# Kernel optimization log

Hardware: AMD Instinct MI355X
Metric: run time of the kernel (lower is better)

## Reference

```python
import jax, jax.numpy as jnp
import numpy as np

N, D = 1024, 256


def setup_inputs() -> dict:
    key = jax.random.key(0)
    k1, k2, k3, k4, k5 = jax.random.split(key, 5)
    s1 = 1.0 / np.sqrt(2 * D)  # fan_in of first linear
    s2 = 1.0 / np.sqrt(D)      # fan_in of second linear
    return {
        "nodes": jax.random.normal(k1, (N, D), dtype=jnp.float32),
        "W1": jax.random.normal(k2, (D, 2 * D), dtype=jnp.float32) * s1,
        "b1": jax.random.normal(k3, (D,), dtype=jnp.float32) * s1,
        "W2": jax.random.normal(k4, (1, D), dtype=jnp.float32) * s2,
        "b2": jax.random.normal(k5, (1,), dtype=jnp.float32) * s2,
    }


def reference(nodes, W1, b1, W2, b2):
    # Original: pair = cat([n_i, n_j], -1); A = sigmoid(Linear2(relu(Linear1(pair))))
    # Algebraically: Linear1(cat(n_i, n_j)) = n_i @ Wa^T + n_j @ Wb^T + b1
    d = nodes.shape[1]
    Wa, Wb = W1[:, :d], W1[:, d:]
    a = nodes @ Wa.T  # (N, D) row-side projection
    b = nodes @ Wb.T  # (N, D) col-side projection
    h = jax.nn.relu(a[:, None, :] + b[None, :, :] + b1)  # (N, N, D)
    logits = jnp.einsum("ijd,d->ij", h, W2[0]) + b2[0]   # (N, N)
    return jax.nn.sigmoid(logits)
```

## Files before the change

### kernel.cpp

```cpp
#include <hip/hip_runtime.h>
#include <math.h>

#define N_NODES 1024
#define DIM     256

typedef float f32x2 __attribute__((ext_vector_type(2)));

__device__ __forceinline__ f32x2 relu2(f32x2 x) {
    return __builtin_elementwise_max(x, (f32x2)0.0f);
}

__global__ __launch_bounds__(256, 2) void k1_gemm(
    const float* __restrict__ nodes, const float* __restrict__ W1,
    const float* __restrict__ b1, float* __restrict__ At, float* __restrict__ Bt)
{
    __shared__ float nt[128][34];
    __shared__ f32x2 wab[DIM][17];

    const int t  = threadIdx.x;
    const int i0 = (blockIdx.x & 31) * 32;
    const int d0 = (blockIdx.x >> 5) * 16;

    {
        const int m = t & 15, s = t >> 4;
        const float* srcA = W1 + (d0 + s) * (2 * DIM);
        const float* srcB = srcA + DIM;
        #pragma unroll
        for (int rep = 0; rep < 4; ++rep) {
            const int k = rep * 64 + m * 4;
            float4 va = *(const float4*)(srcA + k);
            float4 vb = *(const float4*)(srcB + k);
            wab[k+0][s] = f32x2{va.x, vb.x};
            wab[k+1][s] = f32x2{va.y, vb.y};
            wab[k+2][s] = f32x2{va.z, vb.z};
            wab[k+3][s] = f32x2{va.w, vb.w};
        }
    }

    const int tx = t & 15;
    const int ty = t >> 4;
    const int sm = t & 7, ss = t >> 3;
    const float* nsrc = nodes + (i0 + ss) * DIM;

    f32x2 accA = {0.f, 0.f}, accB = {0.f, 0.f};

    for (int kc = 0; kc < DIM; kc += 128) {
        __syncthreads();
        #pragma unroll
        for (int rep = 0; rep < 4; ++rep) {
            const int k = rep * 32 + sm * 4;
            float4 v = *(const float4*)(nsrc + kc + k);
            nt[k+0][ss] = v.x; nt[k+1][ss] = v.y;
            nt[k+2][ss] = v.z; nt[k+3][ss] = v.w;
        }
        __syncthreads();

        #pragma unroll 8
        for (int k = 0; k < 128; ++k) {
            f32x2 av = *(const f32x2*)&nt[k][tx * 2];
            f32x2 wv = wab[kc + k][ty];
            f32x2 waa = __builtin_shufflevector(wv, wv, 0, 0);
            f32x2 wbb = __builtin_shufflevector(wv, wv, 1, 1);
            accA = __builtin_elementwise_fma(av, waa, accA);
            accB = __builtin_elementwise_fma(av, wbb, accB);
        }
    }

    const int d = d0 + ty;
    const int i = i0 + tx * 2;
    const float bb = b1[d];
    f32x2 oa = accA + f32x2{bb, bb};
    *(f32x2*)&At[d * N_NODES + i] = oa;
    *(f32x2*)&Bt[d * N_NODES + i] = accB;
}

__global__ __launch_bounds__(256, 4) void k2_pair(
    const float* __restrict__ At, const float* __restrict__ Bt,
    const float* __restrict__ W2, const float* __restrict__ b2,
    float* __restrict__ out)
{
    __shared__ float As[128][32];
    __shared__ float Bs[128][32];

    const int t  = threadIdx.x;
    const int i0 = (blockIdx.x & 31) * 32;
    const int j0 = (blockIdx.x >> 5) * 32;
    const int tx = t & 15;
    const int ty = t >> 4;

    f32x2 acc0 = {0.f, 0.f};
    f32x2 acc1 = {0.f, 0.f};

    for (int dc = 0; dc < DIM; dc += 128) {
        __syncthreads();
        #pragma unroll
        for (int rep = 0; rep < 4; ++rep) {
            const int flat = rep * 256 + t;
            const int row  = flat >> 3;
            const int c4   = (flat & 7) * 4;
            *(float4*)&As[row][c4] = *(const float4*)(At + (dc+row) * N_NODES + i0 + c4);
            *(float4*)&Bs[row][c4] = *(const float4*)(Bt + (dc+row) * N_NODES + j0 + c4);
        }
        __syncthreads();

        #pragma unroll 8
        for (int d = 0; d < 128; ++d) {
            const float w = W2[dc + d];
            f32x2 wv = {w, w};
            f32x2 a2 = *(const f32x2*)&As[d][ty * 2];
            f32x2 bj = *(const f32x2*)&Bs[d][tx * 2];
            f32x2 axx = __builtin_shufflevector(a2, a2, 0, 0);
            f32x2 ayy = __builtin_shufflevector(a2, a2, 1, 1);
            acc0 = __builtin_elementwise_fma(relu2(axx + bj), wv, acc0);
            acc1 = __builtin_elementwise_fma(relu2(ayy + bj), wv, acc1);
        }
    }

    const float bb = b2[0];
    f32x2 x0 = acc0 + f32x2{bb, bb};
    f32x2 x1 = acc1 + f32x2{bb, bb};
    float2 o0, o1;
    o0.x = 1.0f / (1.0f + __expf(-x0.x));
    o0.y = 1.0f / (1.0f + __expf(-x0.y));
    o1.x = 1.0f / (1.0f + __expf(-x1.x));
    o1.y = 1.0f / (1.0f + __expf(-x1.y));

    const int r = i0 + ty * 2;
    const int c = j0 + tx * 2;
    *(float2*)&out[(r    ) * N_NODES + c] = o0;
    *(float2*)&out[(r + 1) * N_NODES + c] = o1;
}

extern "C" void kernel_launch(void* const* d_in, const int* in_sizes, int n_in,
                              void* d_out, int out_size, void* d_ws, size_t ws_size,
                              hipStream_t stream) {
    const float* nodes = (const float*)d_in[0];
    const float* W1    = (const float*)d_in[1];
    const float* b1    = (const float*)d_in[2];
    const float* W2    = (const float*)d_in[3];
    const float* b2    = (const float*)d_in[4];
    float* out = (float*)d_out;

    float* At = (float*)d_ws;
    float* Bt = At + DIM * N_NODES;

    k1_gemm<<<512,  256, 0, stream>>>(nodes, W1, b1, At, Bt);
    k2_pair<<<1024, 256, 0, stream>>>(At, Bt, W2, b2, out);
}
```

Before: 94.11 us.

## Enlarge pairwise kernel tile to 64x64 with 4x4 outputs per thread

The pairwise relu-reduction kernel now gives each thread a 4x4 block of outputs and each block a 64x64 tile, loaded from LDS as float4 vectors. Each A and B value loaded is reused across more outputs, which lowers LDS traffic per FMA. Output stores widen to float4. The grid shrinks to 256 blocks, roughly one per CU, and the occupancy hint is dropped. That reduces the number of waves available to hide latency.

```diff
diff --git a/kernel.cpp b/kernel.cpp
--- a/kernel.cpp
+++ b/kernel.cpp
@@ -5,6 +5,7 @@
 #define DIM     256
 
 typedef float f32x2 __attribute__((ext_vector_type(2)));
+typedef float f32x4 __attribute__((ext_vector_type(4)));
 
 __device__ __forceinline__ f32x2 relu2(f32x2 x) {
     return __builtin_elementwise_max(x, (f32x2)0.0f);
@@ -74,61 +75,61 @@
     *(f32x2*)&Bt[d * N_NODES + i] = accB;
 }
 
-__global__ __launch_bounds__(256, 4) void k2_pair(
+__global__ __launch_bounds__(256) void k2_pair(
     const float* __restrict__ At, const float* __restrict__ Bt,
     const float* __restrict__ W2, const float* __restrict__ b2,
     float* __restrict__ out)
 {
-    __shared__ float As[128][32];
-    __shared__ float Bs[128][32];
+    __shared__ float As[128][64];
+    __shared__ float Bs[128][64];
 
     const int t  = threadIdx.x;
-    const int i0 = (blockIdx.x & 31) * 32;
-    const int j0 = (blockIdx.x >> 5) * 32;
+    const int i0 = (blockIdx.x & 15) * 64;
+    const int j0 = (blockIdx.x >> 4) * 64;
     const int tx = t & 15;
     const int ty = t >> 4;
 
-    f32x2 acc0 = {0.f, 0.f};
-    f32x2 acc1 = {0.f, 0.f};
+    f32x2 acc[4][2] = {};
 
     for (int dc = 0; dc < DIM; dc += 128) {
         __syncthreads();
         #pragma unroll
-        for (int rep = 0; rep < 4; ++rep) {
+        for (int rep = 0; rep < 8; ++rep) {
             const int flat = rep * 256 + t;
-            const int row  = flat >> 3;
-            const int c4   = (flat & 7) * 4;
+            const int row  = flat >> 4;
+            const int c4   = (flat & 15) * 4;
             *(float4*)&As[row][c4] = *(const float4*)(At + (dc+row) * N_NODES + i0 + c4);
             *(float4*)&Bs[row][c4] = *(const float4*)(Bt + (dc+row) * N_NODES + j0 + c4);
         }
         __syncthreads();
 
-        #pragma unroll 8
+        #pragma unroll 4
         for (int d = 0; d < 128; ++d) {
             const float w = W2[dc + d];
             f32x2 wv = {w, w};
-            f32x2 a2 = *(const f32x2*)&As[d][ty * 2];
-            f32x2 bj = *(const f32x2*)&Bs[d][tx * 2];
-            f32x2 axx = __builtin_shufflevector(a2, a2, 0, 0);
-            f32x2 ayy = __builtin_shufflevector(a2, a2, 1, 1);
-            acc0 = __builtin_elementwise_fma(relu2(axx + bj), wv, acc0);
-            acc1 = __builtin_elementwise_fma(relu2(ayy + bj), wv, acc1);
+            f32x4 a4 = *(const f32x4*)&As[d][ty * 4];
+            f32x4 b4 = *(const f32x4*)&Bs[d][tx * 4];
+            f32x2 b01 = __builtin_shufflevector(b4, b4, 0, 1);
+            f32x2 b23 = __builtin_shufflevector(b4, b4, 2, 3);
+            #pragma unroll
+            for (int r = 0; r < 4; ++r) {
+                f32x2 ar = { a4[r], a4[r] };
+                acc[r][0] = __builtin_elementwise_fma(relu2(ar + b01), wv, acc[r][0]);
+                acc[r][1] = __builtin_elementwise_fma(relu2(ar + b23), wv, acc[r][1]);
+            }
         }
     }
 
     const float bb = b2[0];
-    f32x2 x0 = acc0 + f32x2{bb, bb};
-    f32x2 x1 = acc1 + f32x2{bb, bb};
-    float2 o0, o1;
-    o0.x = 1.0f / (1.0f + __expf(-x0.x));
-    o0.y = 1.0f / (1.0f + __expf(-x0.y));
-    o1.x = 1.0f / (1.0f + __expf(-x1.x));
-    o1.y = 1.0f / (1.0f + __expf(-x1.y));
-
-    const int r = i0 + ty * 2;
-    const int c = j0 + tx * 2;
-    *(float2*)&out[(r    ) * N_NODES + c] = o0;
-    *(float2*)&out[(r + 1) * N_NODES + c] = o1;
+    #pragma unroll
+    for (int r = 0; r < 4; ++r) {
+        float4 o;
+        o.x = 1.0f / (1.0f + __expf(-(acc[r][0].x + bb)));
+        o.y = 1.0f / (1.0f + __expf(-(acc[r][0].y + bb)));
+        o.z = 1.0f / (1.0f + __expf(-(acc[r][1].x + bb)));
+        o.w = 1.0f / (1.0f + __expf(-(acc[r][1].y + bb)));
+        *(float4*)&out[(i0 + ty*4 + r) * N_NODES + j0 + tx*4] = o;
+    }
 }
 
 extern "C" void kernel_launch(void* const* d_in, const int* in_sizes, int n_in,
@@ -144,6 +145,6 @@
     float* At = (float*)d_ws;
     float* Bt = At + DIM * N_NODES;
 
-    k1_gemm<<<512,  256, 0, stream>>>(nodes, W1, b1, At, Bt);
-    k2_pair<<<1024, 256, 0, stream>>>(At, Bt, W2, b2, out);
+    k1_gemm<<<512, 256, 0, stream>>>(nodes, W1, b1, At, Bt);
+    k2_pair<<<256, 256, 0, stream>>>(At, Bt, W2, b2, out);
 }
```

New measurement: 100.9 us. +7.2%, slower.

## Store projections in fp16 and use packed-half add/relu with fdot2 in pair kernel

Applied to the files above, without the earlier changes.

The first kernel now writes the row and column projections as fp16, halving workspace traffic. The pair kernel loads the full 256-dim tile into shared memory at once, interleaving adjacent d-pairs. Its inner loop uses packed half add/max plus v_dot2 fp32 accumulation, so each instruction covers two dims instead of one. This trades fp16 rounding of the pre-activation sums and of W2 for fewer VALU ops, and drops the second load phase and its barriers.

```diff
diff --git a/kernel.cpp b/kernel.cpp
--- a/kernel.cpp
+++ b/kernel.cpp
@@ -5,14 +5,23 @@
 #define DIM     256
 
 typedef float f32x2 __attribute__((ext_vector_type(2)));
+typedef _Float16 f16x2 __attribute__((ext_vector_type(2)));
+typedef unsigned short ushort8 __attribute__((ext_vector_type(8)));
+typedef unsigned int uint2v __attribute__((ext_vector_type(2)));
 
-__device__ __forceinline__ f32x2 relu2(f32x2 x) {
-    return __builtin_elementwise_max(x, (f32x2)0.0f);
+__device__ __forceinline__ f16x2 as_h2(unsigned int u) {
+    union { unsigned int u; f16x2 h; } x; x.u = u; return x.h;
+}
+__device__ __forceinline__ unsigned int as_u32(f16x2 h) {
+    union { unsigned int u; f16x2 h; } x; x.h = h; return x.u;
+}
+__device__ __forceinline__ f16x2 cvt_pkrtz(float a, float b) {
+    return __builtin_bit_cast(f16x2, __builtin_amdgcn_cvt_pkrtz(a, b));
 }
 
 __global__ __launch_bounds__(256, 2) void k1_gemm(
     const float* __restrict__ nodes, const float* __restrict__ W1,
-    const float* __restrict__ b1, float* __restrict__ At, float* __restrict__ Bt)
+    const float* __restrict__ b1, _Float16* __restrict__ Ath, _Float16* __restrict__ Bth)
 {
     __shared__ float nt[128][34];
     __shared__ f32x2 wab[DIM][17];
@@ -69,61 +78,98 @@
     const int d = d0 + ty;
     const int i = i0 + tx * 2;
     const float bb = b1[d];
-    f32x2 oa = accA + f32x2{bb, bb};
-    *(f32x2*)&At[d * N_NODES + i] = oa;
-    *(f32x2*)&Bt[d * N_NODES + i] = accB;
+    f16x2 ha = cvt_pkrtz(accA.x + bb, accA.y + bb);
+    f16x2 hb = cvt_pkrtz(accB.x, accB.y);
+    *(f16x2*)&Ath[d * N_NODES + i] = ha;
+    *(f16x2*)&Bth[d * N_NODES + i] = hb;
 }
 
 __global__ __launch_bounds__(256, 4) void k2_pair(
-    const float* __restrict__ At, const float* __restrict__ Bt,
+    const _Float16* __restrict__ Ath, const _Float16* __restrict__ Bth,
     const float* __restrict__ W2, const float* __restrict__ b2,
     float* __restrict__ out)
 {
-    __shared__ float As[128][32];
-    __shared__ float Bs[128][32];
+    __shared__ unsigned int As2[128 * 34];
+    __shared__ unsigned int Bs2[128 * 34];
+    __shared__ unsigned int w2s[128];
 
     const int t  = threadIdx.x;
     const int i0 = (blockIdx.x & 31) * 32;
     const int j0 = (blockIdx.x >> 5) * 32;
+
+    if (t < 128) {
+        f16x2 wp = cvt_pkrtz(W2[2*t], W2[2*t + 1]);
+        w2s[t] = as_u32(wp);
+    }
+
+    {
+        const int dp = t >> 1;
+        const int ih = (t & 1) * 16;
+        const int base = dp * 34 + ih;
+
+        const _Float16* ra0 = Ath + (2*dp) * N_NODES + i0 + ih;
+        const _Float16* ra1 = ra0 + N_NODES;
+        ushort8 al0 = *(const ushort8*)(ra0);
+        ushort8 al1 = *(const ushort8*)(ra0 + 8);
+        ushort8 ah0 = *(const ushort8*)(ra1);
+        ushort8 ah1 = *(const ushort8*)(ra1 + 8);
+
+        const _Float16* rb0 = Bth + (2*dp) * N_NODES + j0 + ih;
+        const _Float16* rb1 = rb0 + N_NODES;
+        ushort8 bl0 = *(const ushort8*)(rb0);
+        ushort8 bl1 = *(const ushort8*)(rb0 + 8);
+        ushort8 bh0 = *(const ushort8*)(rb1);
+        ushort8 bh1 = *(const ushort8*)(rb1 + 8);
+
+        unsigned int pa[16], pb[16];
+        #pragma unroll
+        for (int k = 0; k < 8; ++k) {
+            pa[k]   = (unsigned int)al0[k] | ((unsigned int)ah0[k] << 16);
+            pa[k+8] = (unsigned int)al1[k] | ((unsigned int)ah1[k] << 16);
+            pb[k]   = (unsigned int)bl0[k] | ((unsigned int)bh0[k] << 16);
+            pb[k+8] = (unsigned int)bl1[k] | ((unsigned int)bh1[k] << 16);
+        }
+        #pragma unroll
+        for (int k = 0; k < 16; k += 2) {
+            *(uint2v*)&As2[base + k] = uint2v{pa[k], pa[k+1]};
+            *(uint2v*)&Bs2[base + k] = uint2v{pb[k], pb[k+1]};
+        }
+    }
+    __syncthreads();
+
     const int tx = t & 15;
     const int ty = t >> 4;
+    float acc00 = 0.f, acc01 = 0.f, acc10 = 0.f, acc11 = 0.f;
 
-    f32x2 acc0 = {0.f, 0.f};
-    f32x2 acc1 = {0.f, 0.f};
+    const unsigned int* pa = As2 + ty * 2;
+    const unsigned int* pb = Bs2 + tx * 2;
+    const f16x2 hz = (f16x2)(_Float16)0.0f;
 
-    for (int dc = 0; dc < DIM; dc += 128) {
-        __syncthreads();
-        #pragma unroll
-        for (int rep = 0; rep < 4; ++rep) {
-            const int flat = rep * 256 + t;
-            const int row  = flat >> 3;
-            const int c4   = (flat & 7) * 4;
-            *(float4*)&As[row][c4] = *(const float4*)(At + (dc+row) * N_NODES + i0 + c4);
-            *(float4*)&Bs[row][c4] = *(const float4*)(Bt + (dc+row) * N_NODES + j0 + c4);
-        }
-        __syncthreads();
+    #pragma unroll 8
+    for (int dp = 0; dp < 128; ++dp) {
+        uint2v av = *(const uint2v*)(pa + dp * 34);
+        uint2v bv = *(const uint2v*)(pb + dp * 34);
+        f16x2 wp = as_h2(w2s[dp]);
+        f16x2 a0 = as_h2(av[0]), a1 = as_h2(av[1]);
+        f16x2 b0 = as_h2(bv[0]), b1v = as_h2(bv[1]);
 
-        #pragma unroll 8
-        for (int d = 0; d < 128; ++d) {
-            const float w = W2[dc + d];
-            f32x2 wv = {w, w};
-            f32x2 a2 = *(const f32x2*)&As[d][ty * 2];
-            f32x2 bj = *(const f32x2*)&Bs[d][tx * 2];
-            f32x2 axx = __builtin_shufflevector(a2, a2, 0, 0);
-            f32x2 ayy = __builtin_shufflevector(a2, a2, 1, 1);
-            acc0 = __builtin_elementwise_fma(relu2(axx + bj), wv, acc0);
-            acc1 = __builtin_elementwise_fma(relu2(ayy + bj), wv, acc1);
-        }
+        f16x2 h;
+        h = __builtin_elementwise_max(a0 + b0,  hz);
+        acc00 = __builtin_amdgcn_fdot2(h, wp, acc00, false);
+        h = __builtin_elementwise_max(a0 + b1v, hz);
+        acc01 = __builtin_amdgcn_fdot2(h, wp, acc01, false);
+        h = __builtin_elementwise_max(a1 + b0,  hz);
+        acc10 = __builtin_amdgcn_fdot2(h, wp, acc10, false);
+        h = __builtin_elementwise_max(a1 + b1v, hz);
+        acc11 = __builtin_amdgcn_fdot2(h, wp, acc11, false);
     }
 
     const float bb = b2[0];
-    f32x2 x0 = acc0 + f32x2{bb, bb};
-    f32x2 x1 = acc1 + f32x2{bb, bb};
     float2 o0, o1;
-    o0.x = 1.0f / (1.0f + __expf(-x0.x));
-    o0.y = 1.0f / (1.0f + __expf(-x0.y));
-    o1.x = 1.0f / (1.0f + __expf(-x1.x));
-    o1.y = 1.0f / (1.0f + __expf(-x1.y));
+    o0.x = 1.0f / (1.0f + __expf(-(acc00 + bb)));
+    o0.y = 1.0f / (1.0f + __expf(-(acc01 + bb)));
+    o1.x = 1.0f / (1.0f + __expf(-(acc10 + bb)));
+    o1.y = 1.0f / (1.0f + __expf(-(acc11 + bb)));
 
     const int r = i0 + ty * 2;
     const int c = j0 + tx * 2;
@@ -141,9 +187,9 @@
     const float* b2    = (const float*)d_in[4];
     float* out = (float*)d_out;
 
-    float* At = (float*)d_ws;
-    float* Bt = At + DIM * N_NODES;
+    _Float16* Ath = (_Float16*)d_ws;
+    _Float16* Bth = Ath + DIM * N_NODES;
 
-    k1_gemm<<<512,  256, 0, stream>>>(nodes, W1, b1, At, Bt);
-    k2_pair<<<1024, 256, 0, stream>>>(At, Bt, W2, b2, out);
+    k1_gemm<<<512,  256, 0, stream>>>(nodes, W1, b1, Ath, Bth);
+    k2_pair<<<1024, 256, 0, stream>>>(Ath, Bth, W2, b2, out);
 }
```

New measurement: 88.20 us. 1.07x faster.
